# Kernel tuning notes

Measured on AMD Instinct MI355X. Metric: run time of the kernel, lower is better.

The kernel has to match this reference:

```python
import jax, jax.numpy as jnp
import numpy as np

B, N, D, H = 4, 4096, 1024, 16
HD = D // H

def setup_inputs() -> dict:
    key = jax.random.key(0)
    k1, k2, k3, k4 = jax.random.split(key, 4)
    x = jax.random.normal(k1, (B, N, D), dtype=jnp.float32)
    rotary_pos = jax.random.normal(k2, (B, N, D, 2), dtype=jnp.float32)
    W_qkv = jax.random.normal(k3, (3 * D, D), dtype=jnp.float32) * (D ** -0.5)
    W_out = jax.random.normal(k4, (D, D), dtype=jnp.float32) * (D ** -0.5)
    b_out = jnp.zeros((D,), dtype=jnp.float32)
    return {"x": x, "rotary_pos": rotary_pos, "W_qkv": W_qkv, "W_out": W_out, "b_out": b_out}

def _embed_rotary(x, cos, sin):
    # x, cos, sin: [B, H, N, HD]; rotate interleaved pairs
    x2 = jnp.stack([-x[..., 1::2], x[..., 0::2]], axis=-1).reshape(x.shape)
    return x * cos + x2 * sin

def reference(x, rotary_pos, W_qkv, W_out, b_out):
    b, n, d = x.shape
    qkv = jnp.einsum('bnd,ed->bne', x, W_qkv)            # [B, N, 3D]
    qkv = qkv.reshape(b, n, 3, H, HD).transpose(2, 0, 3, 1, 4)  # [3, B, H, N, HD]
    q, k, v = qkv[0], qkv[1], qkv[2]
    cos = rotary_pos[..., 0].reshape(b, n, H, HD).transpose(0, 2, 1, 3)  # [B, H, N, HD]
    sin = rotary_pos[..., 1].reshape(b, n, H, HD).transpose(0, 2, 1, 3)
    q = _embed_rotary(q, cos, sin)
    k = _embed_rotary(k, cos, sin)
    scale = HD ** -0.5
    scores = jnp.einsum('bhqd,bhkd->bhqk', q, k) * scale  # [B, H, N, N]
    attn = jax.nn.softmax(scores, axis=-1)
    out = jnp.einsum('bhqk,bhkd->bhqd', attn, v)          # [B, H, N, HD]
    out = out.transpose(0, 2, 1, 3).reshape(b, n, d)      # [B, N, D]
    return out @ W_out.T + b_out
```

## Files before the change

### kernel.cpp

```cpp
#include <hip/hip_runtime.h>
#include <hip/hip_bf16.h>
#include <stdint.h>
#include <stddef.h>

typedef __attribute__((ext_vector_type(8))) __bf16 bf16x8;
typedef __attribute__((ext_vector_type(4))) float f32x4;
typedef __attribute__((ext_vector_type(16))) float f32x16;

#define MFMA16(a, b, c) __builtin_amdgcn_mfma_f32_16x16x32_bf16((a), (b), (c), 0, 0, 0)
#define MFMA32(a, b, c) __builtin_amdgcn_mfma_f32_32x32x16_bf16((a), (b), (c), 0, 0, 0)

static constexpr int Bc = 4, Nc = 4096, Dc = 1024, Hc = 16, HDc = 64;

__device__ __forceinline__ uint16_t f2bf(float f) {
  __bf16 h = (__bf16)f;
  return __builtin_bit_cast(uint16_t, h);
}

__device__ __forceinline__ float fexp2(float x) {
#if __has_builtin(__builtin_amdgcn_exp2f)
  return __builtin_amdgcn_exp2f(x);
#else
  return __builtin_exp2f(x);
#endif
}

__device__ __forceinline__ void gload16(const void* g, void* l) {
  __builtin_amdgcn_global_load_lds(
      (__attribute__((address_space(1))) void*)(g),
      (__attribute__((address_space(3))) void*)(l), 16, 0, 0);
}

__global__ __launch_bounds__(256) void cvt_f32_bf16(
    const float* __restrict__ src, uint16_t* __restrict__ dst, int n) {
  const int i = (blockIdx.x * 256 + threadIdx.x) * 8;
  if (i >= n) return;
  const float4 a = *(const float4*)(src + i);
  const float4 b = *(const float4*)(src + i + 4);
  union { uint16_t u[8]; uint4 v; } o;
  o.u[0] = f2bf(a.x); o.u[1] = f2bf(a.y); o.u[2] = f2bf(a.z); o.u[3] = f2bf(a.w);
  o.u[4] = f2bf(b.x); o.u[5] = f2bf(b.y); o.u[6] = f2bf(b.z); o.u[7] = f2bf(b.w);
  *(uint4*)(dst + i) = o.v;
}

template <int EPI>
__global__ __launch_bounds__(256, 2) void gemm_bt(
    const uint16_t* __restrict__ A, const uint16_t* __restrict__ Bw, int K,
    const float* __restrict__ rot, uint16_t* __restrict__ Qb,
    uint16_t* __restrict__ Kb, uint16_t* __restrict__ Vg,
    const float* __restrict__ bias, float* __restrict__ Out) {
  __shared__ __align__(16) uint16_t As[128 * 64];
  __shared__ __align__(16) uint16_t Bs[128 * 64];
  const int tid = threadIdx.x;
  const int lane = tid & 63, wave = tid >> 6;
  const int l15 = lane & 15, g = lane >> 4;
  const int wr = wave >> 1, wc = wave & 1;
  const int m0 = blockIdx.y * 128;
  const int n0 = blockIdx.x * 128;

  f32x4 acc[4][4];
  const f32x4 fz = {0.f, 0.f, 0.f, 0.f};
#pragma unroll
  for (int i = 0; i < 4; ++i)
#pragma unroll
    for (int j = 0; j < 4; ++j) acc[i][j] = fz;

  for (int kt = 0; kt < K; kt += 64) {
    __syncthreads();
#pragma unroll
    for (int i = 0; i < 4; ++i) {
      const int chunk = tid + i * 256;
      const int r = chunk >> 3, c = chunk & 7;
      const int cs = c ^ (r & 7);
      gload16(A + (size_t)(m0 + r) * K + kt + cs * 8, &As[chunk * 8]);
      gload16(Bw + (size_t)(n0 + r) * K + kt + cs * 8, &Bs[chunk * 8]);
    }
    __syncthreads();

    bf16x8 af[4][2], bfr[4][2];
#pragma unroll
    for (int mi = 0; mi < 4; ++mi)
#pragma unroll
      for (int kk = 0; kk < 2; ++kk) {
        const int r = wr * 64 + mi * 16 + l15;
        const int ca = (kk * 4 + g) ^ (r & 7);
        af[mi][kk] = *(const bf16x8*)((const char*)As + r * 128 + ca * 16);
        const int r2 = wc * 64 + mi * 16 + l15;
        const int cb = (kk * 4 + g) ^ (r2 & 7);
        bfr[mi][kk] = *(const bf16x8*)((const char*)Bs + r2 * 128 + cb * 16);
      }
#pragma unroll
    for (int mi = 0; mi < 4; ++mi)
#pragma unroll
      for (int nj = 0; nj < 4; ++nj)
#pragma unroll
        for (int kk = 0; kk < 2; ++kk)
          acc[mi][nj] = MFMA16(af[mi][kk], bfr[nj][kk], acc[mi][nj]);
  }

  if (EPI == 0) {
    const int b = m0 >> 12;
#pragma unroll
    for (int nj = 0; nj < 4; ++nj) {
      const int e = n0 + wc * 64 + nj * 16 + l15;
      const int part = e >> 10;
      const int d = e & 1023;
      const int h = d >> 6, hd = d & 63;
      const float sc = (part == 0) ? 0.18033688011112042f : 1.0f;
#pragma unroll
      for (int mi = 0; mi < 4; ++mi) {
        if (part == 2) {
          const int nb = (m0 & 4095) + wr * 64 + mi * 16 + g * 4;
          const int vv = nb & 63;
          const int pos = (nb & ~63) + (2 * (vv >> 4) + ((vv >> 2) & 1)) * 8 +
                          ((vv >> 3) & 1) * 4;
          uint2 pv;
          pv.x = (uint32_t)f2bf(acc[mi][nj][0]) |
                 ((uint32_t)f2bf(acc[mi][nj][1]) << 16);
          pv.y = (uint32_t)f2bf(acc[mi][nj][2]) |
                 ((uint32_t)f2bf(acc[mi][nj][3]) << 16);
          *(uint2*)(Vg + ((size_t)(b * Hc + h) * HDc + hd) * Nc + pos) = pv;
        } else {
          uint16_t* dst = (part == 0) ? Qb : Kb;
          const size_t base = ((size_t)(b * Hc + h) * Nc) * HDc + hd;
#pragma unroll
          for (int rg = 0; rg < 4; ++rg) {
            const int m = m0 + wr * 64 + mi * 16 + g * 4 + rg;
            const int n = m & (Nc - 1);
            const float val = acc[mi][nj][rg];
            const float partner = __shfl_xor(val, 1);
            const float x2 = (e & 1) ? partner : -partner;
            const float2 cs =
                *(const float2*)(rot + ((size_t)(b * Nc + n) * Dc + d) * 2);
            dst[base + (size_t)n * HDc] = f2bf((val * cs.x + x2 * cs.y) * sc);
          }
        }
      }
    }
  } else {
#pragma unroll
    for (int nj = 0; nj < 4; ++nj) {
      const int e = n0 + wc * 64 + nj * 16 + l15;
      const float bia = bias[e];
#pragma unroll
      for (int mi = 0; mi < 4; ++mi)
#pragma unroll
        for (int rg = 0; rg < 4; ++rg) {
          const int m = m0 + wr * 64 + mi * 16 + g * 4 + rg;
          Out[(size_t)m * Dc + e] = acc[mi][nj][rg] + bia;
        }
    }
  }
}

__global__ __launch_bounds__(256, 3) void attn_fa(
    const uint16_t* __restrict__ Qb, const uint16_t* __restrict__ Kb,
    const uint16_t* __restrict__ Vg, uint16_t* __restrict__ Ob) {
  __shared__ __align__(16) uint16_t Ks[2][64 * 64];
  __shared__ __align__(16) uint16_t Vt[2][64 * 64];
  const int tid = threadIdx.x;
  const int lane = tid & 63, wave = tid >> 6;
  const int l31 = lane & 31, hi = lane >> 5;
  const int sw = l31 & 7;
  const int id = blockIdx.x;
  const int kk2 = id >> 3;
  const int bh = (id & 7) + 8 * (kk2 >> 5);
  const int q0 = (kk2 & 31) * 128;
  const size_t bhN = (size_t)bh * Nc;
  const size_t bhHD = (size_t)bh * HDc;
  const int ph = (id * 23) & 63;

  bf16x8 qf[4];
#pragma unroll
  for (int ks = 0; ks < 4; ++ks)
    qf[ks] = *(const bf16x8*)(Qb + (bhN + q0 + wave * 32 + l31) * HDc +
                              ks * 16 + hi * 8);

  const f32x16 fzv = {};

  f32x16 O16[2] = {{}, {}};
  float lrow = 0.f;

  bf16x8 paP[4], vfP[2][4];
  {
    const bf16x8 bz = {};
#pragma unroll
    for (int m = 0; m < 4; ++m) { paP[m] = bz; vfP[0][m] = bz; vfP[1][m] = bz; }
  }

  auto stage = [&](uint16_t* ksd, uint16_t* vtd, int tile) {
    const int kv0 = tile * 64;
#pragma unroll
    for (int i = 0; i < 2; ++i) {
      const int ch = tid + i * 256;
      const int r = ch >> 3, c = ch & 7;
      const int cs = c ^ (r & 7);
      gload16(Kb + (bhN + kv0 + r) * HDc + cs * 8, ksd + ch * 8);
      gload16(Vg + (bhHD + r) * Nc + kv0 + cs * 8, vtd + ch * 8);
    }
  };

  stage(Ks[0], Vt[0], ph);
  int cur = 0;
  for (int t = 0; t < Nc / 64; ++t) {
    __syncthreads();
    if (t < Nc / 64 - 1)
      stage(Ks[cur ^ 1], Vt[cur ^ 1], (ph + t + 1) & 63);

    const uint16_t* ksp = &Ks[cur][0];
    const uint16_t* vtp = &Vt[cur][0];

    __builtin_amdgcn_s_setprio(1);
#pragma unroll
    for (int df = 0; df < 2; ++df)
#pragma unroll
      for (int m = 0; m < 4; ++m)
        O16[df] = MFMA32(vfP[df][m], paP[m], O16[df]);

    f32x16 St[2];
#pragma unroll
    for (int c = 0; c < 2; ++c) {
      {
        bf16x8 kf = *(const bf16x8*)(&ksp[(c * 32 + l31) * 64 + ((hi ^ sw) * 8)]);
        St[c] = MFMA32(kf, qf[0], fzv);
      }
#pragma unroll
      for (int ks = 1; ks < 4; ++ks) {
        bf16x8 kf = *(const bf16x8*)(&ksp[(c * 32 + l31) * 64 +
                                          (((ks * 2 + hi) ^ sw) * 8)]);
        St[c] = MFMA32(kf, qf[ks], St[c]);
      }
    }
    __builtin_amdgcn_s_setprio(0);

#pragma unroll
    for (int r = 0; r < 16; ++r) {
      St[0][r] = fexp2(St[0][r]);
      St[1][r] = fexp2(St[1][r]);
    }

    {
      f32x16 sv = St[0] + St[1];
      f32x4 s4;
#pragma unroll
      for (int j = 0; j < 4; ++j)
        s4[j] = (sv[j] + sv[j + 4]) + (sv[j + 8] + sv[j + 12]);
      lrow += (s4[0] + s4[1]) + (s4[2] + s4[3]);
    }

#pragma unroll
    for (int m = 0; m < 4; ++m) {
      const int c = m >> 1, rr = (m & 1) * 2;
#pragma unroll
      for (int j = 0; j < 4; ++j) {
        paP[m][j] = (__bf16)St[c][rr * 4 + j];
        paP[m][j + 4] = (__bf16)St[c][rr * 4 + 4 + j];
      }
    }

#pragma unroll
    for (int df = 0; df < 2; ++df) {
      const int drow = df * 32 + l31;
#pragma unroll
      for (int m = 0; m < 4; ++m)
        vfP[df][m] = *(const bf16x8*)(&vtp[drow * 64 + (((2 * m + hi) ^ sw) * 8)]);
    }
    cur ^= 1;
  }

#pragma unroll
  for (int df = 0; df < 2; ++df)
#pragma unroll
    for (int m = 0; m < 4; ++m)
      O16[df] = MFMA32(vfP[df][m], paP[m], O16[df]);

  lrow += __shfl_xor(lrow, 32);
  const int b = bh >> 4, h = bh & 15;
  const float inv = 1.f / lrow;
  const int n = q0 + wave * 32 + l31;
  uint16_t* orow = Ob + ((size_t)b * Nc + n) * Dc + h * HDc;
#pragma unroll
  for (int df = 0; df < 2; ++df)
#pragma unroll
    for (int r2 = 0; r2 < 4; ++r2) {
      uint2 pv;
      pv.x = (uint32_t)f2bf(O16[df][r2 * 4 + 0] * inv) |
             ((uint32_t)f2bf(O16[df][r2 * 4 + 1] * inv) << 16);
      pv.y = (uint32_t)f2bf(O16[df][r2 * 4 + 2] * inv) |
             ((uint32_t)f2bf(O16[df][r2 * 4 + 3] * inv) << 16);
      *(uint2*)(orow + df * 32 + r2 * 8 + hi * 4) = pv;
    }
}

extern "C" void kernel_launch(void* const* d_in, const int* in_sizes, int n_in,
                              void* d_out, int out_size, void* d_ws, size_t ws_size,
                              hipStream_t stream) {
  const float* x = (const float*)d_in[0];
  const float* rot = (const float*)d_in[1];
  const float* Wqkv = (const float*)d_in[2];
  const float* Wout = (const float*)d_in[3];
  const float* bout = (const float*)d_in[4];
  float* out = (float*)d_out;

  uint16_t* ws = (uint16_t*)d_ws;
  const size_t XSZ = (size_t)Bc * Nc * Dc;
  const size_t W1SZ = (size_t)3 * Dc * Dc;
  const size_t W2SZ = (size_t)Dc * Dc;
  uint16_t* xb = ws;
  uint16_t* At = ws;
  uint16_t* Qb = ws + XSZ;
  uint16_t* Kb = ws + 2 * XSZ;
  uint16_t* Vg = ws + 3 * XSZ;
  uint16_t* Wqb = ws + 4 * XSZ;
  uint16_t* Wob = ws + 4 * XSZ + W1SZ;

  dim3 blk(256);
  cvt_f32_bf16<<<dim3((XSZ / 8 + 255) / 256), blk, 0, stream>>>(x, xb, (int)XSZ);
  cvt_f32_bf16<<<dim3((W1SZ / 8 + 255) / 256), blk, 0, stream>>>(Wqkv, Wqb, (int)W1SZ);
  cvt_f32_bf16<<<dim3((W2SZ / 8 + 255) / 256), blk, 0, stream>>>(Wout, Wob, (int)W2SZ);

  gemm_bt<0><<<dim3((3 * Dc) / 128, (Bc * Nc) / 128), blk, 0, stream>>>(
      xb, Wqb, Dc, rot, Qb, Kb, Vg, nullptr, nullptr);
  attn_fa<<<dim3((Nc / 128) * (Bc * Hc)), blk, 0, stream>>>(Qb, Kb, Vg, At);
  gemm_bt<1><<<dim3(Dc / 128, (Bc * Nc) / 128), blk, 0, stream>>>(
      At, Wob, Dc, nullptr, nullptr, nullptr, nullptr, bout, out);
}
```

Measured before the change: 546.4 us.

## Double-buffer GEMM LDS tiles, merge conversion kernels, drop attention KV phase offset

```diff
diff --git a/kernel.cpp b/kernel.cpp
--- a/kernel.cpp
+++ b/kernel.cpp
@@ -11,6 +11,9 @@
 #define MFMA32(a, b, c) __builtin_amdgcn_mfma_f32_32x32x16_bf16((a), (b), (c), 0, 0, 0)
 
 static constexpr int Bc = 4, Nc = 4096, Dc = 1024, Hc = 16, HDc = 64;
+static constexpr size_t XSZ = (size_t)Bc * Nc * Dc;
+static constexpr size_t W1SZ = (size_t)3 * Dc * Dc;
+static constexpr size_t W2SZ = (size_t)Dc * Dc;
 
 __device__ __forceinline__ uint16_t f2bf(float f) {
   __bf16 h = (__bf16)f;
@@ -31,16 +34,29 @@
       (__attribute__((address_space(3))) void*)(l), 16, 0, 0);
 }
 
-__global__ __launch_bounds__(256) void cvt_f32_bf16(
-    const float* __restrict__ src, uint16_t* __restrict__ dst, int n) {
-  const int i = (blockIdx.x * 256 + threadIdx.x) * 8;
-  if (i >= n) return;
-  const float4 a = *(const float4*)(src + i);
-  const float4 b = *(const float4*)(src + i + 4);
+__global__ __launch_bounds__(256) void cvt_all(
+    const float* __restrict__ x, const float* __restrict__ w1,
+    const float* __restrict__ w2, uint16_t* __restrict__ xb,
+    uint16_t* __restrict__ w1b, uint16_t* __restrict__ w2b) {
+  const size_t XN = XSZ / 8, W1N = W1SZ / 8, W2N = W2SZ / 8;
+  size_t i = (size_t)blockIdx.x * 256 + threadIdx.x;
+  const float* src;
+  uint16_t* dst;
+  if (i < XN) {
+    src = x; dst = xb;
+  } else if (i < XN + W1N) {
+    src = w1; dst = w1b; i -= XN;
+  } else if (i < XN + W1N + W2N) {
+    src = w2; dst = w2b; i -= XN + W1N;
+  } else {
+    return;
+  }
+  const float4 a = *(const float4*)(src + i * 8);
+  const float4 b = *(const float4*)(src + i * 8 + 4);
   union { uint16_t u[8]; uint4 v; } o;
   o.u[0] = f2bf(a.x); o.u[1] = f2bf(a.y); o.u[2] = f2bf(a.z); o.u[3] = f2bf(a.w);
   o.u[4] = f2bf(b.x); o.u[5] = f2bf(b.y); o.u[6] = f2bf(b.z); o.u[7] = f2bf(b.w);
-  *(uint4*)(dst + i) = o.v;
+  *(uint4*)(dst + i * 8) = o.v;
 }
 
 template <int EPI>
@@ -49,8 +65,8 @@
     const float* __restrict__ rot, uint16_t* __restrict__ Qb,
     uint16_t* __restrict__ Kb, uint16_t* __restrict__ Vg,
     const float* __restrict__ bias, float* __restrict__ Out) {
-  __shared__ __align__(16) uint16_t As[128 * 64];
-  __shared__ __align__(16) uint16_t Bs[128 * 64];
+  __shared__ __align__(16) uint16_t As[2][128 * 64];
+  __shared__ __align__(16) uint16_t Bs[2][128 * 64];
   const int tid = threadIdx.x;
   const int lane = tid & 63, wave = tid >> 6;
   const int l15 = lane & 15, g = lane >> 4;
@@ -65,17 +81,22 @@
 #pragma unroll
     for (int j = 0; j < 4; ++j) acc[i][j] = fz;
 
-  for (int kt = 0; kt < K; kt += 64) {
-    __syncthreads();
+  auto stageg = [&](int buf, int kt) {
 #pragma unroll
     for (int i = 0; i < 4; ++i) {
       const int chunk = tid + i * 256;
       const int r = chunk >> 3, c = chunk & 7;
       const int cs = c ^ (r & 7);
-      gload16(A + (size_t)(m0 + r) * K + kt + cs * 8, &As[chunk * 8]);
-      gload16(Bw + (size_t)(n0 + r) * K + kt + cs * 8, &Bs[chunk * 8]);
-    }
+      gload16(A + (size_t)(m0 + r) * K + kt + cs * 8, &As[buf][chunk * 8]);
+      gload16(Bw + (size_t)(n0 + r) * K + kt + cs * 8, &Bs[buf][chunk * 8]);
+    }
+  };
+
+  stageg(0, 0);
+  int cur = 0;
+  for (int kt = 0; kt < K; kt += 64) {
     __syncthreads();
+    if (kt + 64 < K) stageg(cur ^ 1, kt + 64);
 
     bf16x8 af[4][2], bfr[4][2];
 #pragma unroll
@@ -84,11 +105,12 @@
       for (int kk = 0; kk < 2; ++kk) {
         const int r = wr * 64 + mi * 16 + l15;
         const int ca = (kk * 4 + g) ^ (r & 7);
-        af[mi][kk] = *(const bf16x8*)((const char*)As + r * 128 + ca * 16);
+        af[mi][kk] = *(const bf16x8*)((const char*)&As[cur][0] + r * 128 + ca * 16);
         const int r2 = wc * 64 + mi * 16 + l15;
         const int cb = (kk * 4 + g) ^ (r2 & 7);
-        bfr[mi][kk] = *(const bf16x8*)((const char*)Bs + r2 * 128 + cb * 16);
-      }
+        bfr[mi][kk] = *(const bf16x8*)((const char*)&Bs[cur][0] + r2 * 128 + cb * 16);
+      }
+    __builtin_amdgcn_s_setprio(1);
 #pragma unroll
     for (int mi = 0; mi < 4; ++mi)
 #pragma unroll
@@ -96,6 +118,8 @@
 #pragma unroll
         for (int kk = 0; kk < 2; ++kk)
           acc[mi][nj] = MFMA16(af[mi][kk], bfr[nj][kk], acc[mi][nj]);
+    __builtin_amdgcn_s_setprio(0);
+    cur ^= 1;
   }
 
   if (EPI == 0) {
@@ -168,7 +192,6 @@
   const int q0 = (kk2 & 31) * 128;
   const size_t bhN = (size_t)bh * Nc;
   const size_t bhHD = (size_t)bh * HDc;
-  const int ph = (id * 23) & 63;
 
   bf16x8 qf[4];
 #pragma unroll
@@ -200,12 +223,11 @@
     }
   };
 
-  stage(Ks[0], Vt[0], ph);
+  stage(Ks[0], Vt[0], 0);
   int cur = 0;
   for (int t = 0; t < Nc / 64; ++t) {
     __syncthreads();
-    if (t < Nc / 64 - 1)
-      stage(Ks[cur ^ 1], Vt[cur ^ 1], (ph + t + 1) & 63);
+    if (t < Nc / 64 - 1) stage(Ks[cur ^ 1], Vt[cur ^ 1], t + 1);
 
     const uint16_t* ksp = &Ks[cur][0];
     const uint16_t* vtp = &Vt[cur][0];
@@ -303,9 +325,6 @@
   float* out = (float*)d_out;
 
   uint16_t* ws = (uint16_t*)d_ws;
-  const size_t XSZ = (size_t)Bc * Nc * Dc;
-  const size_t W1SZ = (size_t)3 * Dc * Dc;
-  const size_t W2SZ = (size_t)Dc * Dc;
   uint16_t* xb = ws;
   uint16_t* At = ws;
   uint16_t* Qb = ws + XSZ;
@@ -315,9 +334,9 @@
   uint16_t* Wob = ws + 4 * XSZ + W1SZ;
 
   dim3 blk(256);
-  cvt_f32_bf16<<<dim3((XSZ / 8 + 255) / 256), blk, 0, stream>>>(x, xb, (int)XSZ);
-  cvt_f32_bf16<<<dim3((W1SZ / 8 + 255) / 256), blk, 0, stream>>>(Wqkv, Wqb, (int)W1SZ);
-  cvt_f32_bf16<<<dim3((W2SZ / 8 + 255) / 256), blk, 0, stream>>>(Wout, Wob, (int)W2SZ);
+  const size_t CVN = XSZ / 8 + W1SZ / 8 + W2SZ / 8;
+  cvt_all<<<dim3((unsigned)((CVN + 255) / 256)), blk, 0, stream>>>(
+      x, Wqkv, Wout, xb, Wqb, Wob);
 
   gemm_bt<0><<<dim3((3 * Dc) / 128, (Bc * Nc) / 128), blk, 0, stream>>>(
       xb, Wqb, Dc, rot, Qb, Kb, Vg, nullptr, nullptr);
```

After: 558.8 us. 2.3% more time.
